# Performance work log

Measured on AMD Instinct MI355X. Metric: run time of the kernel, lower is better.

## Reference

```python
import jax, jax.numpy as jnp
import numpy as np

B, K, D = 16384, 64, 128


def setup_inputs() -> dict:
    key = jax.random.key(0)
    kx, kc = jax.random.split(key)
    x = jax.random.normal(kx, (B, D), dtype=jnp.float32)
    centers = jax.random.uniform(kc, (K, D), dtype=jnp.float32)  # torch.rand init
    return {"x": x, "centers": centers}


def reference(x, centers):
    batch, dim = x.shape
    k = centers.shape[0]
    # pairwise squared distances, same math as sum((x - c)^2)
    diff = x[:, None, :] - centers[None, :, :]          # [B, K, D]
    dist_sq = jnp.sum(diff * diff, axis=-1)             # [B, K]
    expo = -0.5 * dist_sq
    # safe softmax over clusters (identical to max-subtracted exp/sum)
    resp = jax.nn.softmax(expo, axis=-1)                # [B, K]
    log_resp = jnp.log(jnp.clip(resp, 1e-8))
    # hard assignment and per-cluster statistics
    assign = jnp.argmin(dist_sq, axis=-1)               # [B] int
    onehot = jax.nn.one_hot(assign, k, dtype=x.dtype)   # [B, K]
    cluster_weight = jnp.sum(onehot, axis=0)            # [K]
    emp_total = jnp.einsum('nk,nd->kd', onehot, x)      # [K, D]
    emp_mean = emp_total / (cluster_weight[:, None] + 1e-7)
    # masked centered samples: onehot[n,k]*(x_n - mean_k) is nonzero only at k=assign(n)
    xm = x - emp_mean[assign]                           # [B, D]
    covar_total = jnp.einsum('nk,nd,ne->kde', onehot, xm, xm)  # [K, D, D]
    covar = covar_total / (cluster_weight[:, None, None] + 1e-7)
    eye = jnp.eye(dim, dtype=x.dtype)
    covar_diag = covar * eye
    covar_off = covar * (1.0 - eye)
    diag_dist_sq = jnp.sum((covar_diag - eye) ** 2, axis=(1, 2))  # [K]
    off_dist_sq = jnp.sum(covar_off ** 2, axis=(1, 2))            # [K]
    mean_dist_sq = jnp.sum((emp_mean - centers) ** 2, axis=1)     # [K]
    mean_mse = jnp.sum(cluster_weight * mean_dist_sq) / (batch * dim)
    covar_mse = jnp.sum(
        cluster_weight * diag_dist_sq / (batch * dim)
        + cluster_weight * off_dist_sq / (batch * dim * (dim - 1.0))
    )
    return log_resp, mean_mse, covar_mse
```

## Files before the change

### kernel.cpp

```cpp
#include <hip/hip_runtime.h>

#define BB 16384
#define KK 64
#define DD 128
#define SEG 128
#define MAXITEMS 192
#define NRB 4
#define RSLAB 4096
#define RBLKS (KK * NRB)

typedef __attribute__((ext_vector_type(8))) short bf16x8;
typedef __attribute__((ext_vector_type(4))) float f32x4;

__device__ __forceinline__ unsigned int packbf2(float a, float b) {
    unsigned ua = __float_as_uint(a);
    unsigned ub = __float_as_uint(b);
    ua = (ua + 0x7FFFu + ((ua >> 16) & 1u)) >> 16;
    ub = (ub + 0x7FFFu + ((ub >> 16) & 1u)) >> 16;
    return ua | (ub << 16);
}

__global__ __launch_bounds__(512) void k_rows(
    const float* __restrict__ x, const float* __restrict__ centers,
    float* __restrict__ log_resp, int* __restrict__ assign,
    int* __restrict__ bhist, int* __restrict__ counter)
{
    __shared__ float xs[64][132];
    __shared__ float ct[DD][66];
    __shared__ float cn2[KK];
    __shared__ int   lh[KK];

    const int tid = threadIdx.x;
    const int row0 = blockIdx.x * 64;

    if (blockIdx.x == 0 && tid == 0) *counter = 0;
    if (tid < KK) lh[tid] = 0;

    for (int g = tid; g < 64 * 32; g += 512) {
        int r = g >> 5, c4 = g & 31;
        float4 v = ((const float4*)(x + (size_t)(row0 + r) * DD))[c4];
        *(float4*)&xs[r][c4 * 4] = v;
    }
    for (int g = tid; g < KK * 32; g += 512) {
        int k = g >> 5, c4 = g & 31;
        float4 v = ((const float4*)(centers + (size_t)k * DD))[c4];
        ct[c4 * 4 + 0][k] = v.x;
        ct[c4 * 4 + 1][k] = v.y;
        ct[c4 * 4 + 2][k] = v.z;
        ct[c4 * 4 + 3][k] = v.w;
    }
    __syncthreads();
    if (tid < KK) {
        float s = 0.f;
        for (int d = 0; d < DD; ++d) { float c = ct[d][tid]; s = fmaf(c, c, s); }
        cn2[tid] = s;
    }
    __syncthreads();

    const int tr = tid >> 5;
    const int tc = tid & 31;
    const int k0 = tc * 2, k1 = k0 + 1;

    float acc0[4], acc1[4];
    #pragma unroll
    for (int i = 0; i < 4; ++i) { acc0[i] = 0.f; acc1[i] = 0.f; }

    for (int d = 0; d < DD; d += 4) {
        float2 b0 = *(const float2*)&ct[d + 0][k0];
        float2 b1 = *(const float2*)&ct[d + 1][k0];
        float2 b2 = *(const float2*)&ct[d + 2][k0];
        float2 b3 = *(const float2*)&ct[d + 3][k0];
        #pragma unroll
        for (int i = 0; i < 4; ++i) {
            float4 a = *(const float4*)&xs[tr * 4 + i][d];
            acc0[i] = fmaf(a.x, b0.x, acc0[i]);
            acc1[i] = fmaf(a.x, b0.y, acc1[i]);
            acc0[i] = fmaf(a.y, b1.x, acc0[i]);
            acc1[i] = fmaf(a.y, b1.y, acc1[i]);
            acc0[i] = fmaf(a.z, b2.x, acc0[i]);
            acc1[i] = fmaf(a.z, b2.y, acc1[i]);
            acc0[i] = fmaf(a.w, b3.x, acc0[i]);
            acc1[i] = fmaf(a.w, b3.y, acc1[i]);
        }
    }

    const float cn0 = 0.5f * cn2[k0], cn1 = 0.5f * cn2[k1];
    #pragma unroll
    for (int i = 0; i < 4; ++i) {
        int row = row0 + tr * 4 + i;
        float v0 = acc0[i] - cn0;
        float v1 = acc1[i] - cn1;
        float m; int idx;
        if (v1 > v0) { m = v1; idx = k1; } else { m = v0; idx = k0; }
        #pragma unroll
        for (int off = 1; off < 32; off <<= 1) {
            float ov = __shfl_xor(m, off);
            int   oi = __shfl_xor(idx, off);
            if (ov > m || (ov == m && oi < idx)) { m = ov; idx = oi; }
        }
        float s = expf(v0 - m) + expf(v1 - m);
        #pragma unroll
        for (int off = 1; off < 32; off <<= 1) s += __shfl_xor(s, off);
        float ls = logf(s);
        float lr0 = fmaxf(v0 - m - ls, -18.4206807f);
        float lr1 = fmaxf(v1 - m - ls, -18.4206807f);
        *(float2*)&log_resp[(size_t)row * KK + k0] = make_float2(lr0, lr1);
        if (tc == 0) {
            assign[row] = idx;
            atomicAdd(&lh[idx], 1);
        }
    }
    __syncthreads();
    if (tid < KK) bhist[blockIdx.x * KK + tid] = lh[tid];
}

__global__ __launch_bounds__(256) void k_scat(
    const int* __restrict__ assign, const int* __restrict__ bhist,
    int* __restrict__ sorted, float* __restrict__ cw,
    int4* __restrict__ items, int* __restrict__ item_count,
    int* __restrict__ ist, int* __restrict__ ien)
{
    __shared__ int ph_tot[4][KK], ph_pre[4][KK];
    __shared__ int cnt_s[KK], pre_s[KK], base_s[KK], cur_s[KK];
    __shared__ int iof[KK + 1];

    const int tid = threadIdx.x;
    const int b = blockIdx.x;
    const int t = tid & 63, q = tid >> 6;

    int tot = 0, pre = 0;
    const int bb0 = q * 64;
    for (int bb = bb0; bb < bb0 + 64; ++bb) {
        int v = bhist[bb * KK + t];
        tot += v;
        if (bb < b) pre += v;
    }
    ph_tot[q][t] = tot; ph_pre[q][t] = pre;
    __syncthreads();

    if (tid < KK) {
        cnt_s[tid] = ph_tot[0][tid] + ph_tot[1][tid] + ph_tot[2][tid] + ph_tot[3][tid];
        pre_s[tid] = ph_pre[0][tid] + ph_pre[1][tid] + ph_pre[2][tid] + ph_pre[3][tid];
        cur_s[tid] = 0;
    }
    __syncthreads();
    if (tid == 0) {
        int base = 0;
        for (int k = 0; k < KK; ++k) { base_s[k] = base; base += cnt_s[k]; }
    }
    __syncthreads();

    if (tid < 64) {
        int r = b * 64 + tid;
        int a = assign[r];
        int p = base_s[a] + pre_s[a] + atomicAdd(&cur_s[a], 1);
        sorted[p] = r;
    }

    if (b == 0) {
        if (tid < KK) cw[tid] = (float)cnt_s[tid];
        if (tid == 0) {
            int ic = 0;
            for (int k = 0; k < KK; ++k) {
                iof[k] = ic;
                ic += (cnt_s[k] + SEG - 1) / SEG;
            }
            iof[KK] = ic;
            *item_count = ic;
        }
        __syncthreads();
        if (tid < KK) {
            const int k = tid, c = cnt_s[k], io = iof[k];
            ist[k] = io;
            ien[k] = iof[k + 1];
            int j = 0;
            for (int s = 0; s < c; s += SEG, ++j) {
                int4 it; it.x = k; it.y = base_s[k] + s;
                it.z = min(SEG, c - s); it.w = 0;
                items[io + j] = it;
            }
        }
    }
}

__global__ __launch_bounds__(256) void k_seg(
    const float* __restrict__ x, const int* __restrict__ sorted,
    const int4* __restrict__ items, const int* __restrict__ item_count,
    float* __restrict__ part, float* __restrict__ emp_part)
{
    if ((int)blockIdx.x >= *item_count) return;
    int4 it = items[blockIdx.x];
    const int gstart = it.y, len = it.z;

    __shared__ int rows_s[128];
    __shared__ unsigned int XT[DD][68];

    const int tid = threadIdx.x;
    const int w = tid >> 6, lane = tid & 63;
    const int c4 = lane & 15, q = lane >> 4;

    f32x4 acc[2][8];
    #pragma unroll
    for (int h = 0; h < 2; ++h)
        #pragma unroll
        for (int nt = 0; nt < 8; ++nt)
            acc[h][nt] = (f32x4){0.f, 0.f, 0.f, 0.f};
    float colsum = 0.f;

    for (int half = 0; half < 2; ++half) {
        const int hoff = half * 128;
        const int hlen = min(128, len - hoff);
        if (hlen <= 0) break;

        __syncthreads();
        if (tid < hlen) rows_s[tid] = sorted[gstart + hoff + tid];
        __syncthreads();

        {
            const int r0 = 2 * lane, r1 = 2 * lane + 1;
            const int d0 = w * 32;
            const float* p0 = x + (size_t)rows_s[r0 < hlen ? r0 : 0] * DD + d0;
            const float* p1 = x + (size_t)rows_s[r1 < hlen ? r1 : 0] * DD + d0;
            #pragma unroll
            for (int i = 0; i < 8; ++i) {
                float4 a = make_float4(0.f, 0.f, 0.f, 0.f);
                float4 b = make_float4(0.f, 0.f, 0.f, 0.f);
                if (r0 < hlen) a = *(const float4*)(p0 + 4 * i);
                if (r1 < hlen) b = *(const float4*)(p1 + 4 * i);
                XT[d0 + 4 * i + 0][lane] = packbf2(a.x, b.x);
                XT[d0 + 4 * i + 1][lane] = packbf2(a.y, b.y);
                XT[d0 + 4 * i + 2][lane] = packbf2(a.z, b.z);
                XT[d0 + 4 * i + 3][lane] = packbf2(a.w, b.w);
            }
        }
        __syncthreads();

        if (tid < DD) {
            float s = 0.f;
            #pragma unroll
            for (int j4 = 0; j4 < 16; ++j4) {
                uint4 v = *(const uint4*)&XT[tid][j4 * 4];
                s += __uint_as_float(v.x << 16) + __uint_as_float(v.x & 0xFFFF0000u);
                s += __uint_as_float(v.y << 16) + __uint_as_float(v.y & 0xFFFF0000u);
                s += __uint_as_float(v.z << 16) + __uint_as_float(v.z & 0xFFFF0000u);
                s += __uint_as_float(v.w << 16) + __uint_as_float(v.w & 0xFFFF0000u);
            }
            colsum += s;
        }

        #pragma unroll
        for (int c = 0; c < 4; ++c) {
            const int ku = c * 16 + q * 4;
            bf16x8 a0 = *(const bf16x8*)&XT[(2 * w + 0) * 16 + c4][ku];
            bf16x8 a1 = *(const bf16x8*)&XT[(2 * w + 1) * 16 + c4][ku];
            #pragma unroll
            for (int nt = 0; nt < 8; ++nt) {
                bf16x8 b = *(const bf16x8*)&XT[nt * 16 + c4][ku];
                acc[0][nt] = __builtin_amdgcn_mfma_f32_16x16x32_bf16(a0, b, acc[0][nt], 0, 0, 0);
                acc[1][nt] = __builtin_amdgcn_mfma_f32_16x16x32_bf16(a1, b, acc[1][nt], 0, 0, 0);
            }
        }
    }

    if (tid < DD) emp_part[blockIdx.x * DD + tid] = colsum;

    float* pb = part + (size_t)blockIdx.x * (DD * DD);
    #pragma unroll
    for (int h = 0; h < 2; ++h) {
        const int m0 = (2 * w + h) * 16 + q * 4;
        #pragma unroll
        for (int nt = 0; nt < 8; ++nt) {
            const int n = nt * 16 + c4;
            pb[(m0 + 0) * DD + n] = acc[h][nt].x;
            pb[(m0 + 1) * DD + n] = acc[h][nt].y;
            pb[(m0 + 2) * DD + n] = acc[h][nt].z;
            pb[(m0 + 3) * DD + n] = acc[h][nt].w;
        }
    }
}

__global__ __launch_bounds__(256) void k_redfinal(
    const float* __restrict__ part, const float* __restrict__ emp_part,
    const float* __restrict__ cw, const float* __restrict__ centers,
    const int* __restrict__ ist, const int* __restrict__ ien,
    float2* __restrict__ spart, int* __restrict__ counter,
    float* __restrict__ outscalars)
{
    const int k = blockIdx.x >> 2;
    const int p = blockIdx.x & 3;
    const int i0 = ist[k], i1 = ien[k];
    const int tid = threadIdx.x;
    const int w = tid >> 6, lane = tid & 63;
    const float wgt = cw[k];
    const float inv = 1.0f / (wgt + 1e-7f);

    __shared__ float mu_s[DD], emp_s[DD];
    __shared__ float emp2[2][DD];
    __shared__ float red[4][RSLAB];

    {
        const int dh = tid & 127, hf = tid >> 7;
        float e0 = 0.f, e1 = 0.f;
        int it = i0 + hf;
        for (; it + 2 < i1; it += 4) {
            e0 += emp_part[it * DD + dh];
            e1 += emp_part[(it + 2) * DD + dh];
        }
        if (it < i1) e0 += emp_part[it * DD + dh];
        emp2[hf][dh] = e0 + e1;
    }
    __syncthreads();
    if (tid < DD) {
        float e = emp2[0][tid] + emp2[1][tid];
        emp_s[tid] = e;
        mu_s[tid] = e * inv;
    }

    float4 acc[16];
    #pragma unroll
    for (int c = 0; c < 16; ++c) acc[c] = make_float4(0.f, 0.f, 0.f, 0.f);

    const int base = p * RSLAB;
    for (int it = i0 + w; it < i1; it += 4) {
        const float* pb = part + (size_t)it * (DD * DD) + base;
        #pragma unroll
        for (int c = 0; c < 16; ++c) {
            float4 v = *(const float4*)&pb[c * 256 + lane * 4];
            acc[c].x += v.x; acc[c].y += v.y; acc[c].z += v.z; acc[c].w += v.w;
        }
    }
    #pragma unroll
    for (int c = 0; c < 16; ++c)
        *(float4*)&red[w][c * 256 + lane * 4] = acc[c];
    __syncthreads();

    float ds = 0.f, os = 0.f, mm = 0.f;
    #pragma unroll
    for (int jj = 0; jj < 16; ++jj) {
        int el = jj * 256 + tid;
        float sx = red[0][el] + red[1][el] + red[2][el] + red[3][el];
        int gel = base + el;
        int d = gel >> 7, e = gel & 127;
        float ctv = sx - mu_s[d] * emp_s[e] - emp_s[d] * mu_s[e]
                  + wgt * mu_s[d] * mu_s[e];
        float v = ctv * inv;
        if (d == e) { float t = v - 1.f; ds += t * t; }
        else        { os += v * v; }
    }
    if (p == 0 && tid < DD) {
        float t = mu_s[tid] - centers[k * DD + tid];
        mm = t * t;
    }

    #pragma unroll
    for (int off = 32; off > 0; off >>= 1) {
        ds += __shfl_down(ds, off);
        os += __shfl_down(os, off);
        mm += __shfl_down(mm, off);
    }
    __shared__ float rds[4], ros[4], rmm[4];
    __shared__ int is_last;
    if (lane == 0) { rds[w] = ds; ros[w] = os; rmm[w] = mm; }
    __syncthreads();
    if (tid == 0) {
        float DS = rds[0] + rds[1] + rds[2] + rds[3];
        float OS = ros[0] + ros[1] + ros[2] + ros[3];
        float MM = rmm[0] + rmm[1] + rmm[2] + rmm[3];
        const float bd = (float)BB * (float)DD;
        float2 mine;
        mine.x = wgt * MM / bd;
        mine.y = wgt * DS / bd + wgt * OS / (bd * (float)(DD - 1));
        spart[blockIdx.x] = mine;
        __threadfence();
        int old = atomicAdd(counter, 1);
        is_last = (old == RBLKS - 1);
    }
    __syncthreads();
    if (is_last) {
        __threadfence();
        float2 v = (tid < RBLKS) ? spart[tid] : make_float2(0.f, 0.f);
        float a = v.x, b = v.y;
        #pragma unroll
        for (int off = 32; off > 0; off >>= 1) {
            a += __shfl_down(a, off);
            b += __shfl_down(b, off);
        }
        __shared__ float ra[4], rb[4];
        if (lane == 0) { ra[w] = a; rb[w] = b; }
        __syncthreads();
        if (tid == 0) {
            outscalars[0] = ra[0] + ra[1] + ra[2] + ra[3];
            outscalars[1] = rb[0] + rb[1] + rb[2] + rb[3];
        }
    }
}

extern "C" void kernel_launch(void* const* d_in, const int* in_sizes, int n_in,
                              void* d_out, int out_size, void* d_ws, size_t ws_size,
                              hipStream_t stream) {
    const float* x = (const float*)d_in[0];
    const float* centers = (const float*)d_in[1];
    float* out = (float*)d_out;
    float* outscalars = out + (size_t)BB * KK;

    char* ws = (char*)d_ws;
    size_t off = 0;
    float*  part     = (float*)(ws + off); off += (size_t)MAXITEMS * DD * DD * 4;
    float*  emp_part = (float*)(ws + off); off += (size_t)MAXITEMS * DD * 4;
    int*    sorted   = (int*)  (ws + off); off += BB * 4;
    int*    assign   = (int*)  (ws + off); off += BB * 4;
    int*    bhist    = (int*)  (ws + off); off += 256 * KK * 4;
    int4*   items    = (int4*) (ws + off); off += 256 * 16;
    float*  cw       = (float*)(ws + off); off += 256;
    int*    itemcnt  = (int*)  (ws + off); off += 256;
    int*    ist      = (int*)  (ws + off); off += 256;
    int*    ien      = (int*)  (ws + off); off += 256;
    float2* spart    = (float2*)(ws + off); off += RBLKS * 8;
    int*    counter  = (int*)  (ws + off); off += 256;

    k_rows    <<<256, 512, 0, stream>>>(x, centers, out, assign, bhist, counter);
    k_scat    <<<256, 256, 0, stream>>>(assign, bhist, sorted, cw, items,
                                        itemcnt, ist, ien);
    k_seg     <<<MAXITEMS, 256, 0, stream>>>(x, sorted, items, itemcnt,
                                             part, emp_part);
    k_redfinal<<<RBLKS, 256, 0, stream>>>(part, emp_part, cw, centers, ist, ien,
                                          spart, counter, outscalars);
}
```

Before: 113.5 us.

## Fuse covariance reduction and final loss into segment kernel via last-arriver pattern

Drops the separate reduction kernel and folds the per-cluster covariance reduction and final scalar sum into the segment kernel. A cluster that fits in one item finishes its statistics straight from MFMA registers and never writes partials. Multi-item clusters use an atomic arrival counter so the last block sums the partials. This removes a kernel launch and most partial-buffer traffic, but the last block per cluster reduces serially with less parallelism.

```diff
diff --git a/kernel.cpp b/kernel.cpp
--- a/kernel.cpp
+++ b/kernel.cpp
@@ -5,9 +5,6 @@
 #define DD 128
 #define SEG 128
 #define MAXITEMS 192
-#define NRB 4
-#define RSLAB 4096
-#define RBLKS (KK * NRB)
 
 typedef __attribute__((ext_vector_type(8))) short bf16x8;
 typedef __attribute__((ext_vector_type(4))) float f32x4;
@@ -23,7 +20,7 @@
 __global__ __launch_bounds__(512) void k_rows(
     const float* __restrict__ x, const float* __restrict__ centers,
     float* __restrict__ log_resp, int* __restrict__ assign,
-    int* __restrict__ bhist, int* __restrict__ counter)
+    int* __restrict__ bhist)
 {
     __shared__ float xs[64][132];
     __shared__ float ct[DD][66];
@@ -33,7 +30,6 @@
     const int tid = threadIdx.x;
     const int row0 = blockIdx.x * 64;
 
-    if (blockIdx.x == 0 && tid == 0) *counter = 0;
     if (tid < KK) lh[tid] = 0;
 
     for (int g = tid; g < 64 * 32; g += 512) {
@@ -118,7 +114,9 @@
     const int* __restrict__ assign, const int* __restrict__ bhist,
     int* __restrict__ sorted, float* __restrict__ cw,
     int4* __restrict__ items, int* __restrict__ item_count,
-    int* __restrict__ ist, int* __restrict__ ien)
+    int* __restrict__ ist, int* __restrict__ ien,
+    int* __restrict__ arrived, int* __restrict__ done_cnt,
+    int* __restrict__ nzp, float2* __restrict__ spart2)
 {
     __shared__ int ph_tot[4][KK], ph_pre[4][KK];
     __shared__ int cnt_s[KK], pre_s[KK], base_s[KK], cur_s[KK];
@@ -158,15 +156,22 @@
     }
 
     if (b == 0) {
-        if (tid < KK) cw[tid] = (float)cnt_s[tid];
+        if (tid < KK) {
+            cw[tid] = (float)cnt_s[tid];
+            arrived[tid] = 0;
+            spart2[tid] = make_float2(0.f, 0.f);
+        }
+        if (tid == KK) *done_cnt = 0;
         if (tid == 0) {
-            int ic = 0;
+            int ic = 0, nzc = 0;
             for (int k = 0; k < KK; ++k) {
                 iof[k] = ic;
                 ic += (cnt_s[k] + SEG - 1) / SEG;
+                nzc += (cnt_s[k] > 0);
             }
             iof[KK] = ic;
             *item_count = ic;
+            *nzp = nzc;
         }
         __syncthreads();
         if (tid < KK) {
@@ -186,14 +191,23 @@
 __global__ __launch_bounds__(256) void k_seg(
     const float* __restrict__ x, const int* __restrict__ sorted,
     const int4* __restrict__ items, const int* __restrict__ item_count,
-    float* __restrict__ part, float* __restrict__ emp_part)
+    const int* __restrict__ ist, const int* __restrict__ ien,
+    const float* __restrict__ cw, const float* __restrict__ centers,
+    float* __restrict__ part, float* __restrict__ emp_part,
+    int* __restrict__ arrived, int* __restrict__ done_cnt,
+    const int* __restrict__ nzp, float2* __restrict__ spart2,
+    float* __restrict__ outscalars)
 {
     if ((int)blockIdx.x >= *item_count) return;
     int4 it = items[blockIdx.x];
-    const int gstart = it.y, len = it.z;
+    const int k = it.x, gstart = it.y, len = it.z;
+    const int i0 = ist[k], i1 = ien[k];
+    const int nitems = i1 - i0;
 
     __shared__ int rows_s[128];
     __shared__ unsigned int XT[DD][68];
+    __shared__ float mu_s[DD], emp_s[DD];
+    __shared__ int ret_s;
 
     const int tid = threadIdx.x;
     const int w = tid >> 6, lane = tid & 63;
@@ -205,153 +219,141 @@
         #pragma unroll
         for (int nt = 0; nt < 8; ++nt)
             acc[h][nt] = (f32x4){0.f, 0.f, 0.f, 0.f};
+
+    if (tid < len) rows_s[tid] = sorted[gstart + tid];
+    __syncthreads();
+
+    {
+        const int r0 = 2 * lane, r1 = 2 * lane + 1;
+        const int d0 = w * 32;
+        const float* p0 = x + (size_t)rows_s[r0 < len ? r0 : 0] * DD + d0;
+        const float* p1 = x + (size_t)rows_s[r1 < len ? r1 : 0] * DD + d0;
+        #pragma unroll
+        for (int i = 0; i < 8; ++i) {
+            float4 a = make_float4(0.f, 0.f, 0.f, 0.f);
+            float4 b = make_float4(0.f, 0.f, 0.f, 0.f);
+            if (r0 < len) a = *(const float4*)(p0 + 4 * i);
+            if (r1 < len) b = *(const float4*)(p1 + 4 * i);
+            XT[d0 + 4 * i + 0][lane] = packbf2(a.x, b.x);
+            XT[d0 + 4 * i + 1][lane] = packbf2(a.y, b.y);
+            XT[d0 + 4 * i + 2][lane] = packbf2(a.z, b.z);
+            XT[d0 + 4 * i + 3][lane] = packbf2(a.w, b.w);
+        }
+    }
+    __syncthreads();
+
     float colsum = 0.f;
-
-    for (int half = 0; half < 2; ++half) {
-        const int hoff = half * 128;
-        const int hlen = min(128, len - hoff);
-        if (hlen <= 0) break;
-
-        __syncthreads();
-        if (tid < hlen) rows_s[tid] = sorted[gstart + hoff + tid];
-        __syncthreads();
-
-        {
-            const int r0 = 2 * lane, r1 = 2 * lane + 1;
-            const int d0 = w * 32;
-            const float* p0 = x + (size_t)rows_s[r0 < hlen ? r0 : 0] * DD + d0;
-            const float* p1 = x + (size_t)rows_s[r1 < hlen ? r1 : 0] * DD + d0;
-            #pragma unroll
-            for (int i = 0; i < 8; ++i) {
-                float4 a = make_float4(0.f, 0.f, 0.f, 0.f);
-                float4 b = make_float4(0.f, 0.f, 0.f, 0.f);
-                if (r0 < hlen) a = *(const float4*)(p0 + 4 * i);
-                if (r1 < hlen) b = *(const float4*)(p1 + 4 * i);
-                XT[d0 + 4 * i + 0][lane] = packbf2(a.x, b.x);
-                XT[d0 + 4 * i + 1][lane] = packbf2(a.y, b.y);
-                XT[d0 + 4 * i + 2][lane] = packbf2(a.z, b.z);
-                XT[d0 + 4 * i + 3][lane] = packbf2(a.w, b.w);
-            }
-        }
-        __syncthreads();
-
-        if (tid < DD) {
-            float s = 0.f;
-            #pragma unroll
-            for (int j4 = 0; j4 < 16; ++j4) {
-                uint4 v = *(const uint4*)&XT[tid][j4 * 4];
-                s += __uint_as_float(v.x << 16) + __uint_as_float(v.x & 0xFFFF0000u);
-                s += __uint_as_float(v.y << 16) + __uint_as_float(v.y & 0xFFFF0000u);
-                s += __uint_as_float(v.z << 16) + __uint_as_float(v.z & 0xFFFF0000u);
-                s += __uint_as_float(v.w << 16) + __uint_as_float(v.w & 0xFFFF0000u);
-            }
-            colsum += s;
-        }
-
-        #pragma unroll
-        for (int c = 0; c < 4; ++c) {
-            const int ku = c * 16 + q * 4;
-            bf16x8 a0 = *(const bf16x8*)&XT[(2 * w + 0) * 16 + c4][ku];
-            bf16x8 a1 = *(const bf16x8*)&XT[(2 * w + 1) * 16 + c4][ku];
+    if (tid < DD) {
+        #pragma unroll
+        for (int j4 = 0; j4 < 16; ++j4) {
+            uint4 v = *(const uint4*)&XT[tid][j4 * 4];
+            colsum += __uint_as_float(v.x << 16) + __uint_as_float(v.x & 0xFFFF0000u);
+            colsum += __uint_as_float(v.y << 16) + __uint_as_float(v.y & 0xFFFF0000u);
+            colsum += __uint_as_float(v.z << 16) + __uint_as_float(v.z & 0xFFFF0000u);
+            colsum += __uint_as_float(v.w << 16) + __uint_as_float(v.w & 0xFFFF0000u);
+        }
+    }
+
+    #pragma unroll
+    for (int c = 0; c < 4; ++c) {
+        const int ku = c * 16 + q * 4;
+        bf16x8 a0 = *(const bf16x8*)&XT[(2 * w + 0) * 16 + c4][ku];
+        bf16x8 a1 = *(const bf16x8*)&XT[(2 * w + 1) * 16 + c4][ku];
+        #pragma unroll
+        for (int nt = 0; nt < 8; ++nt) {
+            bf16x8 b = *(const bf16x8*)&XT[nt * 16 + c4][ku];
+            acc[0][nt] = __builtin_amdgcn_mfma_f32_16x16x32_bf16(a0, b, acc[0][nt], 0, 0, 0);
+            acc[1][nt] = __builtin_amdgcn_mfma_f32_16x16x32_bf16(a1, b, acc[1][nt], 0, 0, 0);
+        }
+    }
+
+    const float wgt = cw[k];
+    const float inv = 1.0f / (wgt + 1e-7f);
+    float ds = 0.f, os = 0.f, mm = 0.f;
+
+    if (nitems == 1) {
+        if (tid < DD) { emp_s[tid] = colsum; mu_s[tid] = colsum * inv; }
+        __syncthreads();
+        #pragma unroll
+        for (int h = 0; h < 2; ++h) {
+            const int m0 = (2 * w + h) * 16 + q * 4;
             #pragma unroll
             for (int nt = 0; nt < 8; ++nt) {
-                bf16x8 b = *(const bf16x8*)&XT[nt * 16 + c4][ku];
-                acc[0][nt] = __builtin_amdgcn_mfma_f32_16x16x32_bf16(a0, b, acc[0][nt], 0, 0, 0);
-                acc[1][nt] = __builtin_amdgcn_mfma_f32_16x16x32_bf16(a1, b, acc[1][nt], 0, 0, 0);
-            }
-        }
-    }
-
-    if (tid < DD) emp_part[blockIdx.x * DD + tid] = colsum;
-
-    float* pb = part + (size_t)blockIdx.x * (DD * DD);
-    #pragma unroll
-    for (int h = 0; h < 2; ++h) {
-        const int m0 = (2 * w + h) * 16 + q * 4;
-        #pragma unroll
-        for (int nt = 0; nt < 8; ++nt) {
-            const int n = nt * 16 + c4;
-            pb[(m0 + 0) * DD + n] = acc[h][nt].x;
-            pb[(m0 + 1) * DD + n] = acc[h][nt].y;
-            pb[(m0 + 2) * DD + n] = acc[h][nt].z;
-            pb[(m0 + 3) * DD + n] = acc[h][nt].w;
-        }
-    }
-}
-
-__global__ __launch_bounds__(256) void k_redfinal(
-    const float* __restrict__ part, const float* __restrict__ emp_part,
-    const float* __restrict__ cw, const float* __restrict__ centers,
-    const int* __restrict__ ist, const int* __restrict__ ien,
-    float2* __restrict__ spart, int* __restrict__ counter,
-    float* __restrict__ outscalars)
-{
-    const int k = blockIdx.x >> 2;
-    const int p = blockIdx.x & 3;
-    const int i0 = ist[k], i1 = ien[k];
-    const int tid = threadIdx.x;
-    const int w = tid >> 6, lane = tid & 63;
-    const float wgt = cw[k];
-    const float inv = 1.0f / (wgt + 1e-7f);
-
-    __shared__ float mu_s[DD], emp_s[DD];
-    __shared__ float emp2[2][DD];
-    __shared__ float red[4][RSLAB];
-
-    {
-        const int dh = tid & 127, hf = tid >> 7;
-        float e0 = 0.f, e1 = 0.f;
-        int it = i0 + hf;
-        for (; it + 2 < i1; it += 4) {
-            e0 += emp_part[it * DD + dh];
-            e1 += emp_part[(it + 2) * DD + dh];
-        }
-        if (it < i1) e0 += emp_part[it * DD + dh];
-        emp2[hf][dh] = e0 + e1;
-    }
-    __syncthreads();
+                const int n = nt * 16 + c4;
+                #pragma unroll
+                for (int j = 0; j < 4; ++j) {
+                    const int d = m0 + j;
+                    float ctv = acc[h][nt][j] - mu_s[d] * emp_s[n] - emp_s[d] * mu_s[n]
+                              + wgt * mu_s[d] * mu_s[n];
+                    float v2 = ctv * inv;
+                    if (d == n) { float tt = v2 - 1.f; ds += tt * tt; }
+                    else        { os += v2 * v2; }
+                }
+            }
+        }
+    } else {
+        if (tid < DD) emp_part[blockIdx.x * DD + tid] = colsum;
+        float* pb = part + (size_t)blockIdx.x * (DD * DD);
+        #pragma unroll
+        for (int h = 0; h < 2; ++h) {
+            const int m0 = (2 * w + h) * 16 + q * 4;
+            #pragma unroll
+            for (int nt = 0; nt < 8; ++nt) {
+                const int n = nt * 16 + c4;
+                pb[(m0 + 0) * DD + n] = acc[h][nt].x;
+                pb[(m0 + 1) * DD + n] = acc[h][nt].y;
+                pb[(m0 + 2) * DD + n] = acc[h][nt].z;
+                pb[(m0 + 3) * DD + n] = acc[h][nt].w;
+            }
+        }
+        __syncthreads();
+        __threadfence();
+        __syncthreads();
+        if (tid == 0) ret_s = atomicAdd(&arrived[k], 1);
+        __syncthreads();
+        if (ret_s != nitems - 1) return;
+        __threadfence();
+
+        if (tid < DD) {
+            float e = 0.f;
+            for (int it2 = i0; it2 < i1; ++it2) e += emp_part[it2 * DD + tid];
+            emp_s[tid] = e;
+            mu_s[tid] = e * inv;
+        }
+        __syncthreads();
+
+        float4 racc[16];
+        #pragma unroll
+        for (int j = 0; j < 16; ++j) racc[j] = make_float4(0.f, 0.f, 0.f, 0.f);
+        for (int it2 = i0; it2 < i1; ++it2) {
+            const float* ppb = part + (size_t)it2 * (DD * DD);
+            #pragma unroll
+            for (int j = 0; j < 16; ++j) {
+                float4 v = *(const float4*)&ppb[j * 1024 + tid * 4];
+                racc[j].x += v.x; racc[j].y += v.y; racc[j].z += v.z; racc[j].w += v.w;
+            }
+        }
+        #pragma unroll
+        for (int j = 0; j < 16; ++j) {
+            const int gel = j * 1024 + tid * 4;
+            const int d = gel >> 7;
+            float sv[4] = {racc[j].x, racc[j].y, racc[j].z, racc[j].w};
+            #pragma unroll
+            for (int c = 0; c < 4; ++c) {
+                const int e = (gel + c) & 127;
+                float ctv = sv[c] - mu_s[d] * emp_s[e] - emp_s[d] * mu_s[e]
+                          + wgt * mu_s[d] * mu_s[e];
+                float v2 = ctv * inv;
+                if (d == e) { float tt = v2 - 1.f; ds += tt * tt; }
+                else        { os += v2 * v2; }
+            }
+        }
+    }
+
     if (tid < DD) {
-        float e = emp2[0][tid] + emp2[1][tid];
-        emp_s[tid] = e;
-        mu_s[tid] = e * inv;
-    }
-
-    float4 acc[16];
-    #pragma unroll
-    for (int c = 0; c < 16; ++c) acc[c] = make_float4(0.f, 0.f, 0.f, 0.f);
-
-    const int base = p * RSLAB;
-    for (int it = i0 + w; it < i1; it += 4) {
-        const float* pb = part + (size_t)it * (DD * DD) + base;
-        #pragma unroll
-        for (int c = 0; c < 16; ++c) {
-            float4 v = *(const float4*)&pb[c * 256 + lane * 4];
-            acc[c].x += v.x; acc[c].y += v.y; acc[c].z += v.z; acc[c].w += v.w;
-        }
-    }
-    #pragma unroll
-    for (int c = 0; c < 16; ++c)
-        *(float4*)&red[w][c * 256 + lane * 4] = acc[c];
-    __syncthreads();
-
-    float ds = 0.f, os = 0.f, mm = 0.f;
-    #pragma unroll
-    for (int jj = 0; jj < 16; ++jj) {
-        int el = jj * 256 + tid;
-        float sx = red[0][el] + red[1][el] + red[2][el] + red[3][el];
-        int gel = base + el;
-        int d = gel >> 7, e = gel & 127;
-        float ctv = sx - mu_s[d] * emp_s[e] - emp_s[d] * mu_s[e]
-                  + wgt * mu_s[d] * mu_s[e];
-        float v = ctv * inv;
-        if (d == e) { float t = v - 1.f; ds += t * t; }
-        else        { os += v * v; }
-    }
-    if (p == 0 && tid < DD) {
-        float t = mu_s[tid] - centers[k * DD + tid];
+        float t = mu_s[tid] - centers[(size_t)k * DD + tid];
         mm = t * t;
     }
-
     #pragma unroll
     for (int off = 32; off > 0; off >>= 1) {
         ds += __shfl_down(ds, off);
@@ -359,7 +361,7 @@
         mm += __shfl_down(mm, off);
     }
     __shared__ float rds[4], ros[4], rmm[4];
-    __shared__ int is_last;
+    __shared__ int last_s;
     if (lane == 0) { rds[w] = ds; ros[w] = os; rmm[w] = mm; }
     __syncthreads();
     if (tid == 0) {
@@ -370,27 +372,23 @@
         float2 mine;
         mine.x = wgt * MM / bd;
         mine.y = wgt * DS / bd + wgt * OS / (bd * (float)(DD - 1));
-        spart[blockIdx.x] = mine;
+        spart2[k] = mine;
         __threadfence();
-        int old = atomicAdd(counter, 1);
-        is_last = (old == RBLKS - 1);
-    }
-    __syncthreads();
-    if (is_last) {
+        int old = atomicAdd(done_cnt, 1);
+        last_s = (old == *nzp - 1);
+    }
+    __syncthreads();
+    if (last_s) {
         __threadfence();
-        float2 v = (tid < RBLKS) ? spart[tid] : make_float2(0.f, 0.f);
-        float a = v.x, b = v.y;
-        #pragma unroll
-        for (int off = 32; off > 0; off >>= 1) {
-            a += __shfl_down(a, off);
-            b += __shfl_down(b, off);
-        }
-        __shared__ float ra[4], rb[4];
-        if (lane == 0) { ra[w] = a; rb[w] = b; }
-        __syncthreads();
-        if (tid == 0) {
-            outscalars[0] = ra[0] + ra[1] + ra[2] + ra[3];
-            outscalars[1] = rb[0] + rb[1] + rb[2] + rb[3];
+        if (w == 0) {
+            float2 v = spart2[lane];
+            float a = v.x, b = v.y;
+            #pragma unroll
+            for (int off = 32; off > 0; off >>= 1) {
+                a += __shfl_down(a, off);
+                b += __shfl_down(b, off);
+            }
+            if (lane == 0) { outscalars[0] = a; outscalars[1] = b; }
         }
     }
 }
@@ -415,14 +413,17 @@
     int*    itemcnt  = (int*)  (ws + off); off += 256;
     int*    ist      = (int*)  (ws + off); off += 256;
     int*    ien      = (int*)  (ws + off); off += 256;
-    float2* spart    = (float2*)(ws + off); off += RBLKS * 8;
-    int*    counter  = (int*)  (ws + off); off += 256;
-
-    k_rows    <<<256, 512, 0, stream>>>(x, centers, out, assign, bhist, counter);
-    k_scat    <<<256, 256, 0, stream>>>(assign, bhist, sorted, cw, items,
-                                        itemcnt, ist, ien);
-    k_seg     <<<MAXITEMS, 256, 0, stream>>>(x, sorted, items, itemcnt,
-                                             part, emp_part);
-    k_redfinal<<<RBLKS, 256, 0, stream>>>(part, emp_part, cw, centers, ist, ien,
-                                          spart, counter, outscalars);
+    int*    arrived  = (int*)  (ws + off); off += KK * 4;
+    int*    done_cnt = (int*)  (ws + off); off += 256;
+    int*    nzp      = (int*)  (ws + off); off += 256;
+    float2* spart2   = (float2*)(ws + off); off += KK * 8;
+
+    k_rows<<<256, 512, 0, stream>>>(x, centers, out, assign, bhist);
+    k_scat<<<256, 256, 0, stream>>>(assign, bhist, sorted, cw, items,
+                                    itemcnt, ist, ien,
+                                    arrived, done_cnt, nzp, spart2);
+    k_seg <<<MAXITEMS, 256, 0, stream>>>(x, sorted, items, itemcnt, ist, ien,
+                                         cw, centers, part, emp_part,
+                                         arrived, done_cnt, nzp, spart2,
+                                         outscalars);
 }
```

Result: slower. 142.3 us (+25.3%).

## Fuse scatter, segment GEMM and reduction into one cooperative kernel

Applied to the files above, without the earlier changes.

The scatter, segment-covariance and final-reduction kernels are merged into one cooperative kernel, with grid-wide syncs between phases. Shared memory becomes a union of the three phase layouts passed as dynamic LDS. Counter reset moves from the row kernel into the scatter phase. This removes two kernel launches and their gaps, at the cost of two grid barriers and a dynamic LDS allocation above 64 KB, which may require gfx950's larger LDS to be usable.

```diff
diff --git a/kernel.cpp b/kernel.cpp
--- a/kernel.cpp
+++ b/kernel.cpp
@@ -1,4 +1,7 @@
 #include <hip/hip_runtime.h>
+#include <hip/hip_cooperative_groups.h>
+
+namespace cg = cooperative_groups;
 
 #define BB 16384
 #define KK 64
@@ -23,7 +26,7 @@
 __global__ __launch_bounds__(512) void k_rows(
     const float* __restrict__ x, const float* __restrict__ centers,
     float* __restrict__ log_resp, int* __restrict__ assign,
-    int* __restrict__ bhist, int* __restrict__ counter)
+    int* __restrict__ bhist)
 {
     __shared__ float xs[64][132];
     __shared__ float ct[DD][66];
@@ -33,7 +36,6 @@
     const int tid = threadIdx.x;
     const int row0 = blockIdx.x * 64;
 
-    if (blockIdx.x == 0 && tid == 0) *counter = 0;
     if (tid < KK) lh[tid] = 0;
 
     for (int g = tid; g < 64 * 32; g += 512) {
@@ -114,283 +116,287 @@
     if (tid < KK) bhist[blockIdx.x * KK + tid] = lh[tid];
 }
 
-__global__ __launch_bounds__(256) void k_scat(
+struct SmemA {
+    int ph_tot[4][KK], ph_pre[4][KK];
+    int cnt_s[KK], pre_s[KK], base_s[KK], cur_s[KK];
+    int iof[KK + 1];
+};
+struct SmemB {
+    int rows_s[128];
+    unsigned int XT[DD][68];
+};
+struct SmemC {
+    float red[4][RSLAB];
+    float mu_s[DD], emp_s[DD];
+    float emp2[2][DD];
+    float rds[4], ros[4], rmm[4];
+    int is_last;
+};
+union SmemU { SmemA a; SmemB b; SmemC c; };
+
+__global__ __launch_bounds__(256) void k_rest(
+    const float* __restrict__ x, const float* __restrict__ centers,
     const int* __restrict__ assign, const int* __restrict__ bhist,
     int* __restrict__ sorted, float* __restrict__ cw,
     int4* __restrict__ items, int* __restrict__ item_count,
-    int* __restrict__ ist, int* __restrict__ ien)
+    int* __restrict__ ist, int* __restrict__ ien,
+    float* __restrict__ part, float* __restrict__ emp_part,
+    float2* __restrict__ spart, int* __restrict__ counter,
+    float* __restrict__ outscalars)
 {
-    __shared__ int ph_tot[4][KK], ph_pre[4][KK];
-    __shared__ int cnt_s[KK], pre_s[KK], base_s[KK], cur_s[KK];
-    __shared__ int iof[KK + 1];
+    extern __shared__ unsigned char smem_raw[];
+    SmemU& smem = *reinterpret_cast<SmemU*>(smem_raw);
+    cg::grid_group grid = cg::this_grid();
 
     const int tid = threadIdx.x;
-    const int b = blockIdx.x;
-    const int t = tid & 63, q = tid >> 6;
-
-    int tot = 0, pre = 0;
-    const int bb0 = q * 64;
-    for (int bb = bb0; bb < bb0 + 64; ++bb) {
-        int v = bhist[bb * KK + t];
-        tot += v;
-        if (bb < b) pre += v;
-    }
-    ph_tot[q][t] = tot; ph_pre[q][t] = pre;
-    __syncthreads();
-
-    if (tid < KK) {
-        cnt_s[tid] = ph_tot[0][tid] + ph_tot[1][tid] + ph_tot[2][tid] + ph_tot[3][tid];
-        pre_s[tid] = ph_pre[0][tid] + ph_pre[1][tid] + ph_pre[2][tid] + ph_pre[3][tid];
-        cur_s[tid] = 0;
-    }
-    __syncthreads();
-    if (tid == 0) {
-        int base = 0;
-        for (int k = 0; k < KK; ++k) { base_s[k] = base; base += cnt_s[k]; }
-    }
-    __syncthreads();
-
-    if (tid < 64) {
-        int r = b * 64 + tid;
-        int a = assign[r];
-        int p = base_s[a] + pre_s[a] + atomicAdd(&cur_s[a], 1);
-        sorted[p] = r;
-    }
-
-    if (b == 0) {
-        if (tid < KK) cw[tid] = (float)cnt_s[tid];
+
+    {
+        const int b = blockIdx.x;
+        const int t = tid & 63, q = tid >> 6;
+
+        int tot = 0, pre = 0;
+        const int bb0 = q * 64;
+        for (int bb = bb0; bb < bb0 + 64; ++bb) {
+            int v = bhist[bb * KK + t];
+            tot += v;
+            if (bb < b) pre += v;
+        }
+        smem.a.ph_tot[q][t] = tot; smem.a.ph_pre[q][t] = pre;
+        __syncthreads();
+
+        if (tid < KK) {
+            smem.a.cnt_s[tid] = smem.a.ph_tot[0][tid] + smem.a.ph_tot[1][tid]
+                              + smem.a.ph_tot[2][tid] + smem.a.ph_tot[3][tid];
+            smem.a.pre_s[tid] = smem.a.ph_pre[0][tid] + smem.a.ph_pre[1][tid]
+                              + smem.a.ph_pre[2][tid] + smem.a.ph_pre[3][tid];
+            smem.a.cur_s[tid] = 0;
+        }
+        __syncthreads();
         if (tid == 0) {
-            int ic = 0;
-            for (int k = 0; k < KK; ++k) {
-                iof[k] = ic;
-                ic += (cnt_s[k] + SEG - 1) / SEG;
-            }
-            iof[KK] = ic;
-            *item_count = ic;
-        }
-        __syncthreads();
-        if (tid < KK) {
-            const int k = tid, c = cnt_s[k], io = iof[k];
-            ist[k] = io;
-            ien[k] = iof[k + 1];
-            int j = 0;
-            for (int s = 0; s < c; s += SEG, ++j) {
-                int4 it; it.x = k; it.y = base_s[k] + s;
-                it.z = min(SEG, c - s); it.w = 0;
-                items[io + j] = it;
-            }
-        }
-    }
-}
-
-__global__ __launch_bounds__(256) void k_seg(
-    const float* __restrict__ x, const int* __restrict__ sorted,
-    const int4* __restrict__ items, const int* __restrict__ item_count,
-    float* __restrict__ part, float* __restrict__ emp_part)
-{
-    if ((int)blockIdx.x >= *item_count) return;
-    int4 it = items[blockIdx.x];
-    const int gstart = it.y, len = it.z;
-
-    __shared__ int rows_s[128];
-    __shared__ unsigned int XT[DD][68];
-
-    const int tid = threadIdx.x;
-    const int w = tid >> 6, lane = tid & 63;
-    const int c4 = lane & 15, q = lane >> 4;
-
-    f32x4 acc[2][8];
-    #pragma unroll
-    for (int h = 0; h < 2; ++h)
-        #pragma unroll
-        for (int nt = 0; nt < 8; ++nt)
-            acc[h][nt] = (f32x4){0.f, 0.f, 0.f, 0.f};
-    float colsum = 0.f;
-
-    for (int half = 0; half < 2; ++half) {
-        const int hoff = half * 128;
-        const int hlen = min(128, len - hoff);
-        if (hlen <= 0) break;
-
-        __syncthreads();
-        if (tid < hlen) rows_s[tid] = sorted[gstart + hoff + tid];
+            int base = 0;
+            for (int k = 0; k < KK; ++k) { smem.a.base_s[k] = base; base += smem.a.cnt_s[k]; }
+        }
+        __syncthreads();
+
+        if (tid < 64) {
+            int r = b * 64 + tid;
+            int a = assign[r];
+            int p = smem.a.base_s[a] + smem.a.pre_s[a] + atomicAdd(&smem.a.cur_s[a], 1);
+            sorted[p] = r;
+        }
+
+        if (b == 0) {
+            if (tid < KK) cw[tid] = (float)smem.a.cnt_s[tid];
+            if (tid == KK) *counter = 0;
+            if (tid == 0) {
+                int ic = 0;
+                for (int k = 0; k < KK; ++k) {
+                    smem.a.iof[k] = ic;
+                    ic += (smem.a.cnt_s[k] + SEG - 1) / SEG;
+                }
+                smem.a.iof[KK] = ic;
+                *item_count = ic;
+            }
+            __syncthreads();
+            if (tid < KK) {
+                const int k = tid, c = smem.a.cnt_s[k], io = smem.a.iof[k];
+                ist[k] = io;
+                ien[k] = smem.a.iof[k + 1];
+                int j = 0;
+                for (int s = 0; s < c; s += SEG, ++j) {
+                    int4 it; it.x = k; it.y = smem.a.base_s[k] + s;
+                    it.z = min(SEG, c - s); it.w = 0;
+                    items[io + j] = it;
+                }
+            }
+        }
+    }
+
+    __threadfence();
+    grid.sync();
+
+    if ((int)blockIdx.x < *item_count) {
+        int4 it = items[blockIdx.x];
+        const int gstart = it.y, len = it.z;
+
+        const int w = tid >> 6, lane = tid & 63;
+        const int c4 = lane & 15, q = lane >> 4;
+
+        f32x4 acc[2][8];
+        #pragma unroll
+        for (int h = 0; h < 2; ++h)
+            #pragma unroll
+            for (int nt = 0; nt < 8; ++nt)
+                acc[h][nt] = (f32x4){0.f, 0.f, 0.f, 0.f};
+
+        if (tid < len) smem.b.rows_s[tid] = sorted[gstart + tid];
         __syncthreads();
 
         {
             const int r0 = 2 * lane, r1 = 2 * lane + 1;
             const int d0 = w * 32;
-            const float* p0 = x + (size_t)rows_s[r0 < hlen ? r0 : 0] * DD + d0;
-            const float* p1 = x + (size_t)rows_s[r1 < hlen ? r1 : 0] * DD + d0;
+            const float* p0 = x + (size_t)smem.b.rows_s[r0 < len ? r0 : 0] * DD + d0;
+            const float* p1 = x + (size_t)smem.b.rows_s[r1 < len ? r1 : 0] * DD + d0;
             #pragma unroll
             for (int i = 0; i < 8; ++i) {
                 float4 a = make_float4(0.f, 0.f, 0.f, 0.f);
                 float4 b = make_float4(0.f, 0.f, 0.f, 0.f);
-                if (r0 < hlen) a = *(const float4*)(p0 + 4 * i);
-                if (r1 < hlen) b = *(const float4*)(p1 + 4 * i);
-                XT[d0 + 4 * i + 0][lane] = packbf2(a.x, b.x);
-                XT[d0 + 4 * i + 1][lane] = packbf2(a.y, b.y);
-                XT[d0 + 4 * i + 2][lane] = packbf2(a.z, b.z);
-                XT[d0 + 4 * i + 3][lane] = packbf2(a.w, b.w);
-            }
-        }
-        __syncthreads();
-
+                if (r0 < len) a = *(const float4*)(p0 + 4 * i);
+                if (r1 < len) b = *(const float4*)(p1 + 4 * i);
+                smem.b.XT[d0 + 4 * i + 0][lane] = packbf2(a.x, b.x);
+                smem.b.XT[d0 + 4 * i + 1][lane] = packbf2(a.y, b.y);
+                smem.b.XT[d0 + 4 * i + 2][lane] = packbf2(a.z, b.z);
+                smem.b.XT[d0 + 4 * i + 3][lane] = packbf2(a.w, b.w);
+            }
+        }
+        __syncthreads();
+
+        float colsum = 0.f;
         if (tid < DD) {
-            float s = 0.f;
             #pragma unroll
             for (int j4 = 0; j4 < 16; ++j4) {
-                uint4 v = *(const uint4*)&XT[tid][j4 * 4];
-                s += __uint_as_float(v.x << 16) + __uint_as_float(v.x & 0xFFFF0000u);
-                s += __uint_as_float(v.y << 16) + __uint_as_float(v.y & 0xFFFF0000u);
-                s += __uint_as_float(v.z << 16) + __uint_as_float(v.z & 0xFFFF0000u);
-                s += __uint_as_float(v.w << 16) + __uint_as_float(v.w & 0xFFFF0000u);
-            }
-            colsum += s;
+                uint4 v = *(const uint4*)&smem.b.XT[tid][j4 * 4];
+                colsum += __uint_as_float(v.x << 16) + __uint_as_float(v.x & 0xFFFF0000u);
+                colsum += __uint_as_float(v.y << 16) + __uint_as_float(v.y & 0xFFFF0000u);
+                colsum += __uint_as_float(v.z << 16) + __uint_as_float(v.z & 0xFFFF0000u);
+                colsum += __uint_as_float(v.w << 16) + __uint_as_float(v.w & 0xFFFF0000u);
+            }
+            emp_part[blockIdx.x * DD + tid] = colsum;
         }
 
         #pragma unroll
         for (int c = 0; c < 4; ++c) {
             const int ku = c * 16 + q * 4;
-            bf16x8 a0 = *(const bf16x8*)&XT[(2 * w + 0) * 16 + c4][ku];
-            bf16x8 a1 = *(const bf16x8*)&XT[(2 * w + 1) * 16 + c4][ku];
+            bf16x8 a0 = *(const bf16x8*)&smem.b.XT[(2 * w + 0) * 16 + c4][ku];
+            bf16x8 a1 = *(const bf16x8*)&smem.b.XT[(2 * w + 1) * 16 + c4][ku];
             #pragma unroll
             for (int nt = 0; nt < 8; ++nt) {
-                bf16x8 b = *(const bf16x8*)&XT[nt * 16 + c4][ku];
+                bf16x8 b = *(const bf16x8*)&smem.b.XT[nt * 16 + c4][ku];
                 acc[0][nt] = __builtin_amdgcn_mfma_f32_16x16x32_bf16(a0, b, acc[0][nt], 0, 0, 0);
                 acc[1][nt] = __builtin_amdgcn_mfma_f32_16x16x32_bf16(a1, b, acc[1][nt], 0, 0, 0);
             }
         }
-    }
-
-    if (tid < DD) emp_part[blockIdx.x * DD + tid] = colsum;
-
-    float* pb = part + (size_t)blockIdx.x * (DD * DD);
-    #pragma unroll
-    for (int h = 0; h < 2; ++h) {
-        const int m0 = (2 * w + h) * 16 + q * 4;
-        #pragma unroll
-        for (int nt = 0; nt < 8; ++nt) {
-            const int n = nt * 16 + c4;
-            pb[(m0 + 0) * DD + n] = acc[h][nt].x;
-            pb[(m0 + 1) * DD + n] = acc[h][nt].y;
-            pb[(m0 + 2) * DD + n] = acc[h][nt].z;
-            pb[(m0 + 3) * DD + n] = acc[h][nt].w;
-        }
-    }
-}
-
-__global__ __launch_bounds__(256) void k_redfinal(
-    const float* __restrict__ part, const float* __restrict__ emp_part,
-    const float* __restrict__ cw, const float* __restrict__ centers,
-    const int* __restrict__ ist, const int* __restrict__ ien,
-    float2* __restrict__ spart, int* __restrict__ counter,
-    float* __restrict__ outscalars)
-{
-    const int k = blockIdx.x >> 2;
-    const int p = blockIdx.x & 3;
-    const int i0 = ist[k], i1 = ien[k];
-    const int tid = threadIdx.x;
-    const int w = tid >> 6, lane = tid & 63;
-    const float wgt = cw[k];
-    const float inv = 1.0f / (wgt + 1e-7f);
-
-    __shared__ float mu_s[DD], emp_s[DD];
-    __shared__ float emp2[2][DD];
-    __shared__ float red[4][RSLAB];
+
+        float* pb = part + (size_t)blockIdx.x * (DD * DD);
+        #pragma unroll
+        for (int h = 0; h < 2; ++h) {
+            const int m0 = (2 * w + h) * 16 + q * 4;
+            #pragma unroll
+            for (int nt = 0; nt < 8; ++nt) {
+                const int n = nt * 16 + c4;
+                pb[(m0 + 0) * DD + n] = acc[h][nt].x;
+                pb[(m0 + 1) * DD + n] = acc[h][nt].y;
+                pb[(m0 + 2) * DD + n] = acc[h][nt].z;
+                pb[(m0 + 3) * DD + n] = acc[h][nt].w;
+            }
+        }
+    }
+
+    __threadfence();
+    grid.sync();
 
     {
-        const int dh = tid & 127, hf = tid >> 7;
-        float e0 = 0.f, e1 = 0.f;
-        int it = i0 + hf;
-        for (; it + 2 < i1; it += 4) {
-            e0 += emp_part[it * DD + dh];
-            e1 += emp_part[(it + 2) * DD + dh];
-        }
-        if (it < i1) e0 += emp_part[it * DD + dh];
-        emp2[hf][dh] = e0 + e1;
-    }
-    __syncthreads();
-    if (tid < DD) {
-        float e = emp2[0][tid] + emp2[1][tid];
-        emp_s[tid] = e;
-        mu_s[tid] = e * inv;
-    }
-
-    float4 acc[16];
-    #pragma unroll
-    for (int c = 0; c < 16; ++c) acc[c] = make_float4(0.f, 0.f, 0.f, 0.f);
-
-    const int base = p * RSLAB;
-    for (int it = i0 + w; it < i1; it += 4) {
-        const float* pb = part + (size_t)it * (DD * DD) + base;
-        #pragma unroll
-        for (int c = 0; c < 16; ++c) {
-            float4 v = *(const float4*)&pb[c * 256 + lane * 4];
-            acc[c].x += v.x; acc[c].y += v.y; acc[c].z += v.z; acc[c].w += v.w;
-        }
-    }
-    #pragma unroll
-    for (int c = 0; c < 16; ++c)
-        *(float4*)&red[w][c * 256 + lane * 4] = acc[c];
-    __syncthreads();
-
-    float ds = 0.f, os = 0.f, mm = 0.f;
-    #pragma unroll
-    for (int jj = 0; jj < 16; ++jj) {
-        int el = jj * 256 + tid;
-        float sx = red[0][el] + red[1][el] + red[2][el] + red[3][el];
-        int gel = base + el;
-        int d = gel >> 7, e = gel & 127;
-        float ctv = sx - mu_s[d] * emp_s[e] - emp_s[d] * mu_s[e]
-                  + wgt * mu_s[d] * mu_s[e];
-        float v = ctv * inv;
-        if (d == e) { float t = v - 1.f; ds += t * t; }
-        else        { os += v * v; }
-    }
-    if (p == 0 && tid < DD) {
-        float t = mu_s[tid] - centers[k * DD + tid];
-        mm = t * t;
-    }
-
-    #pragma unroll
-    for (int off = 32; off > 0; off >>= 1) {
-        ds += __shfl_down(ds, off);
-        os += __shfl_down(os, off);
-        mm += __shfl_down(mm, off);
-    }
-    __shared__ float rds[4], ros[4], rmm[4];
-    __shared__ int is_last;
-    if (lane == 0) { rds[w] = ds; ros[w] = os; rmm[w] = mm; }
-    __syncthreads();
-    if (tid == 0) {
-        float DS = rds[0] + rds[1] + rds[2] + rds[3];
-        float OS = ros[0] + ros[1] + ros[2] + ros[3];
-        float MM = rmm[0] + rmm[1] + rmm[2] + rmm[3];
-        const float bd = (float)BB * (float)DD;
-        float2 mine;
-        mine.x = wgt * MM / bd;
-        mine.y = wgt * DS / bd + wgt * OS / (bd * (float)(DD - 1));
-        spart[blockIdx.x] = mine;
-        __threadfence();
-        int old = atomicAdd(counter, 1);
-        is_last = (old == RBLKS - 1);
-    }
-    __syncthreads();
-    if (is_last) {
-        __threadfence();
-        float2 v = (tid < RBLKS) ? spart[tid] : make_float2(0.f, 0.f);
-        float a = v.x, b = v.y;
+        const int k = blockIdx.x >> 2;
+        const int p = blockIdx.x & 3;
+        const int i0 = ist[k], i1 = ien[k];
+        const int w = tid >> 6, lane = tid & 63;
+        const float wgt = cw[k];
+        const float inv = 1.0f / (wgt + 1e-7f);
+
+        {
+            const int dh = tid & 127, hf = tid >> 7;
+            float e0 = 0.f, e1 = 0.f;
+            int it = i0 + hf;
+            for (; it + 2 < i1; it += 4) {
+                e0 += emp_part[it * DD + dh];
+                e1 += emp_part[(it + 2) * DD + dh];
+            }
+            if (it < i1) e0 += emp_part[it * DD + dh];
+            smem.c.emp2[hf][dh] = e0 + e1;
+        }
+        __syncthreads();
+        if (tid < DD) {
+            float e = smem.c.emp2[0][tid] + smem.c.emp2[1][tid];
+            smem.c.emp_s[tid] = e;
+            smem.c.mu_s[tid] = e * inv;
+        }
+
+        float4 acc[16];
+        #pragma unroll
+        for (int c = 0; c < 16; ++c) acc[c] = make_float4(0.f, 0.f, 0.f, 0.f);
+
+        const int base = p * RSLAB;
+        for (int it = i0 + w; it < i1; it += 4) {
+            const float* pb = part + (size_t)it * (DD * DD) + base;
+            #pragma unroll
+            for (int c = 0; c < 16; ++c) {
+                float4 v = *(const float4*)&pb[c * 256 + lane * 4];
+                acc[c].x += v.x; acc[c].y += v.y; acc[c].z += v.z; acc[c].w += v.w;
+            }
+        }
+        #pragma unroll
+        for (int c = 0; c < 16; ++c)
+            *(float4*)&smem.c.red[w][c * 256 + lane * 4] = acc[c];
+        __syncthreads();
+
+        float ds = 0.f, os = 0.f, mm = 0.f;
+        #pragma unroll
+        for (int jj = 0; jj < 16; ++jj) {
+            int el = jj * 256 + tid;
+            float sx = smem.c.red[0][el] + smem.c.red[1][el]
+                     + smem.c.red[2][el] + smem.c.red[3][el];
+            int gel = base + el;
+            int d = gel >> 7, e = gel & 127;
+            float ctv = sx - smem.c.mu_s[d] * smem.c.emp_s[e]
+                      - smem.c.emp_s[d] * smem.c.mu_s[e]
+                      + wgt * smem.c.mu_s[d] * smem.c.mu_s[e];
+            float v = ctv * inv;
+            if (d == e) { float t = v - 1.f; ds += t * t; }
+            else        { os += v * v; }
+        }
+        if (p == 0 && tid < DD) {
+            float t = smem.c.mu_s[tid] - centers[k * DD + tid];
+            mm = t * t;
+        }
+
         #pragma unroll
         for (int off = 32; off > 0; off >>= 1) {
-            a += __shfl_down(a, off);
-            b += __shfl_down(b, off);
-        }
-        __shared__ float ra[4], rb[4];
-        if (lane == 0) { ra[w] = a; rb[w] = b; }
+            ds += __shfl_down(ds, off);
+            os += __shfl_down(os, off);
+            mm += __shfl_down(mm, off);
+        }
+        if (lane == 0) { smem.c.rds[w] = ds; smem.c.ros[w] = os; smem.c.rmm[w] = mm; }
         __syncthreads();
         if (tid == 0) {
-            outscalars[0] = ra[0] + ra[1] + ra[2] + ra[3];
-            outscalars[1] = rb[0] + rb[1] + rb[2] + rb[3];
+            float DS = smem.c.rds[0] + smem.c.rds[1] + smem.c.rds[2] + smem.c.rds[3];
+            float OS = smem.c.ros[0] + smem.c.ros[1] + smem.c.ros[2] + smem.c.ros[3];
+            float MM = smem.c.rmm[0] + smem.c.rmm[1] + smem.c.rmm[2] + smem.c.rmm[3];
+            const float bd = (float)BB * (float)DD;
+            float2 mine;
+            mine.x = wgt * MM / bd;
+            mine.y = wgt * DS / bd + wgt * OS / (bd * (float)(DD - 1));
+            spart[blockIdx.x] = mine;
+            __threadfence();
+            int old = atomicAdd(counter, 1);
+            smem.c.is_last = (old == RBLKS - 1);
+        }
+        __syncthreads();
+        if (smem.c.is_last) {
+            __threadfence();
+            float2 v = (tid < RBLKS) ? spart[tid] : make_float2(0.f, 0.f);
+            float a = v.x, b = v.y;
+            #pragma unroll
+            for (int off = 32; off > 0; off >>= 1) {
+                a += __shfl_down(a, off);
+                b += __shfl_down(b, off);
+            }
+            __shared__ float ra[4], rb[4];
+            if (lane == 0) { ra[w] = a; rb[w] = b; }
+            __syncthreads();
+            if (tid == 0) {
+                outscalars[0] = ra[0] + ra[1] + ra[2] + ra[3];
+                outscalars[1] = rb[0] + rb[1] + rb[2] + rb[3];
+            }
         }
     }
 }
@@ -418,11 +424,14 @@
     float2* spart    = (float2*)(ws + off); off += RBLKS * 8;
     int*    counter  = (int*)  (ws + off); off += 256;
 
-    k_rows    <<<256, 512, 0, stream>>>(x, centers, out, assign, bhist, counter);
-    k_scat    <<<256, 256, 0, stream>>>(assign, bhist, sorted, cw, items,
-                                        itemcnt, ist, ien);
-    k_seg     <<<MAXITEMS, 256, 0, stream>>>(x, sorted, items, itemcnt,
-                                             part, emp_part);
-    k_redfinal<<<RBLKS, 256, 0, stream>>>(part, emp_part, cw, centers, ist, ien,
-                                          spart, counter, outscalars);
+    k_rows<<<256, 512, 0, stream>>>(x, centers, out, assign, bhist);
+
+    void* args[] = {
+        (void*)&x, (void*)&centers, (void*)&assign, (void*)&bhist,
+        (void*)&sorted, (void*)&cw, (void*)&items, (void*)&itemcnt,
+        (void*)&ist, (void*)&ien, (void*)&part, (void*)&emp_part,
+        (void*)&spart, (void*)&counter, (void*)&outscalars
+    };
+    hipLaunchCooperativeKernel((const void*)k_rest, dim3(256), dim3(256),
+                               args, (unsigned int)sizeof(SmemU), stream);
 }
```

New measurement: 260.5 us. +129.4%, slower.
